# Performance work log

Hardware: AMD Instinct MI355X
Metric: run time of the kernel (lower is better)

The kernel has to match this reference:

```python
import jax, jax.numpy as jnp
import numpy as np

B, T, C = 1, 2048, 1024
HS = 64
H = C // HS
EPS_GN = 0.00064


def _fwd(x, v_first, x_prev, init_state, x_r, x_w, x_k, x_v, x_a, x_g,
         w0, w1, w2, a0, a1, a2, v0, v1, v2, g1, g2,
         k_k, k_a, r_k, Wr, Wk, Wv, Wo, ln_w, ln_b, cu_seqlens):
    # token shift: previous token, sequence starts replaced by cached state x_prev
    xx = jnp.concatenate([jnp.zeros((1, 1, C), x.dtype), x[:, :-1, :]], axis=1)
    xx = xx.at[0, cu_seqlens[:-1], :].set(x_prev)
    xx = xx - x
    xr = x + xx * x_r
    xw = x + xx * x_w
    xk = x + xx * x_k
    xv = x + xx * x_v
    xa = x + xx * x_a
    xg = x + xx * x_g
    r = xr @ Wr.T
    # log-decay, strictly negative: w = -exp(-softplus(-z) - 0.5)
    w = -jnp.exp(-jax.nn.softplus(-(w0 + jnp.tanh(xw @ w1) @ w2)) - 0.5)
    k = xk @ Wk.T
    v = xv @ Wv.T
    # layer_id != 0: mix toward first-layer value
    v = v + (v_first - v) * jax.nn.sigmoid(v0 + (xv @ v1) @ v2)
    a = jax.nn.sigmoid(a0 + (xa @ a1) @ a2)
    g = jax.nn.sigmoid(xg @ g1) @ g2
    kk = (k * k_k).reshape(B, T, H, HS)
    kk = kk / jnp.maximum(jnp.linalg.norm(kk, axis=-1, keepdims=True), 1e-12)
    k = k * (1.0 + (a - 1.0) * k_a)
    r4 = r.reshape(B, T, H, HS)
    w4 = w.reshape(B, T, H, HS)
    k4 = k.reshape(B, T, H, HS)
    v4 = v.reshape(B, T, H, HS)
    a4 = a.reshape(B, T, H, HS)
    aa = -kk
    bb = kk * a4

    # RWKV-7 selective-decay linear RNN (chunk_rwkv7 semantics):
    #   S_t = S_{t-1} diag(exp(w_t)) + (S_{t-1} a_t) b_t^T + v_t k_t^T ; o_t = S_t r_t
    def step(S, ts):
        r_t, w_t, k_t, v_t, a_t, b_t = ts  # each [H,HS]
        sa = jnp.einsum('hvj,hj->hv', S, a_t)
        S = S * jnp.exp(w_t)[:, None, :] + sa[:, :, None] * b_t[:, None, :] \
            + v_t[:, :, None] * k_t[:, None, :]
        o = jnp.einsum('hvk,hk->hv', S, r_t)
        return S, o

    _, y = jax.lax.scan(step, init_state, (r4[0], w4[0], k4[0], v4[0], aa[0], bb[0]))
    # GroupNorm with num_groups=H over channels, eps=0.00064
    y = y.reshape(B * T, H, HS)
    mu = y.mean(-1, keepdims=True)
    var = ((y - mu) ** 2).mean(-1, keepdims=True)
    yn = (y - mu) / jnp.sqrt(var + EPS_GN)
    yn = yn * ln_w.reshape(H, HS) + ln_b.reshape(H, HS)
    xo = yn.reshape(B, T, C)
    # per-head bonus term
    xo = xo + ((r4 * k4 * r_k).sum(-1, keepdims=True) * v4).reshape(B, T, C)
    return (xo * g) @ Wo.T


def setup_inputs():
    keys = jax.random.split(jax.random.key(0), 32)
    it = iter(range(32))
    def nrm(shape, s=0.02):
        return jax.random.normal(keys[next(it)], shape, dtype=jnp.float32) * s
    inp = {}
    inp['x'] = jax.random.normal(keys[next(it)], (B, T, C), jnp.float32)
    inp['v_first'] = jax.random.normal(keys[next(it)], (B, T, C), jnp.float32)
    inp['x_prev'] = jax.random.normal(keys[next(it)], (1, C), jnp.float32)
    inp['init_state'] = jnp.zeros((H, HS, HS), jnp.float32)
    for nm in ['x_r', 'x_w', 'x_k', 'x_v', 'x_a', 'x_g', 'w0', 'a0', 'v0', 'k_k', 'k_a']:
        inp[nm] = nrm((C,))
    inp['w1'] = nrm((C, 64)); inp['w2'] = nrm((64, C))
    inp['a1'] = nrm((C, 64)); inp['a2'] = nrm((64, C))
    inp['v1'] = nrm((C, 32)); inp['v2'] = nrm((32, C))
    inp['g1'] = nrm((C, 128)); inp['g2'] = nrm((128, C))
    inp['r_k'] = nrm((H, HS))
    inp['Wr'] = nrm((C, C)); inp['Wk'] = nrm((C, C))
    inp['Wv'] = nrm((C, C)); inp['Wo'] = nrm((C, C))
    inp['ln_w'] = jnp.ones((C,), jnp.float32)
    inp['ln_b'] = jnp.zeros((C,), jnp.float32)
    inp['cu_seqlens'] = jnp.array([0, T], dtype=jnp.int32)
    return inp


def reference(x, v_first, x_prev, init_state, x_r, x_w, x_k, x_v, x_a, x_g,
              w0, w1, w2, a0, a1, a2, v0, v1, v2, g1, g2,
              k_k, k_a, r_k, Wr, Wk, Wv, Wo, ln_w, ln_b, cu_seqlens):
    return _fwd(x, v_first, x_prev, init_state, x_r, x_w, x_k, x_v, x_a, x_g,
                w0, w1, w2, a0, a1, a2, v0, v1, v2, g1, g2,
                k_k, k_a, r_k, Wr, Wk, Wv, Wo, ln_w, ln_b, cu_seqlens)
```

## Files before the change

### kernel.cpp

```cpp
#include <hip/hip_runtime.h>

#define T_LEN 2048
#define C_DIM 1024
#define PAIR_F 768
#define NCH 32
#define CPAIR 32

#define AS1 __attribute__((address_space(1)))
#define AS3 __attribute__((address_space(3)))

typedef __attribute__((ext_vector_type(8))) short bf8_t;
typedef __attribute__((ext_vector_type(4))) float f4_t;
typedef __attribute__((ext_vector_type(2))) float f2_t;

static __device__ __forceinline__ float sigf(float x) {
    return 1.f / (1.f + __expf(-x));
}
static __device__ __forceinline__ unsigned short f2bf(float f) {
    unsigned u = __float_as_uint(f);
    u += 0x7fff + ((u >> 16) & 1);
    return (unsigned short)(u >> 16);
}

static __device__ __forceinline__ float red16(float x) {
    int xi;
    xi = __builtin_amdgcn_mov_dpp(__float_as_int(x), 0x128, 0xf, 0xf, true);
    x += __int_as_float(xi);
    xi = __builtin_amdgcn_mov_dpp(__float_as_int(x), 0x124, 0xf, 0xf, true);
    x += __int_as_float(xi);
    xi = __builtin_amdgcn_mov_dpp(__float_as_int(x), 0x122, 0xf, 0xf, true);
    x += __int_as_float(xi);
    xi = __builtin_amdgcn_mov_dpp(__float_as_int(x), 0x121, 0xf, 0xf, true);
    x += __int_as_float(xi);
    return x;
}
static __device__ __forceinline__ float red64(float x) {
    x = red16(x);
    x += __shfl_xor(x, 16);
    x += __shfl_xor(x, 32);
    return x;
}

static __device__ __forceinline__ f2_t f2bc(float s) { return (f2_t){s, s}; }
static __device__ __forceinline__ f2_t fma2(f2_t a, f2_t b, f2_t c) {
    return __builtin_elementwise_fma(a, b, c);
}
static __device__ __forceinline__ f2_t lo2(const float4& v) { return (f2_t){v.x, v.y}; }
static __device__ __forceinline__ f2_t hi2(const float4& v) { return (f2_t){v.z, v.w}; }

static __device__ __forceinline__ float dot4pk(f2_t Sl, f2_t Sh, const float4& A) {
    f2_t m = Sl * lo2(A);
    m = fma2(Sh, hi2(A), m);
    return m.x + m.y;
}

__global__ __launch_bounds__(256) void wcvtall(
    const float* __restrict__ Wr, const float* __restrict__ Wk,
    const float* __restrict__ Wv, const float* __restrict__ Wo,
    const float* __restrict__ w1, const float* __restrict__ a1,
    const float* __restrict__ v1, const float* __restrict__ g1,
    const float* __restrict__ g2,
    unsigned short* __restrict__ dst, unsigned short* __restrict__ lw16,
    unsigned short* __restrict__ g2t16)
{
    const int b = blockIdx.x;
    if (b < 4096) {
        const size_t idx = ((size_t)b * 256 + threadIdx.x) * 4;
        const int sel = (int)(idx >> 20);
        const float* src = sel == 0 ? Wr : sel == 1 ? Wk : sel == 2 ? Wv : Wo;
        float4 v = *(const float4*)(src + (idx & 0xFFFFF));
        ushort4 o = {f2bf(v.x), f2bf(v.y), f2bf(v.z), f2bf(v.w)};
        *(ushort4*)(dst + idx) = o;
        return;
    }
    if (b >= 4384) {
        const int rr = b - 4384;
        const int i  = rr * 2 + (threadIdx.x >> 7);
        const int c  = threadIdx.x & 127;
        g2t16[(size_t)i * 128 + c] = f2bf(g2[(size_t)c * C_DIM + i]);
        return;
    }
    const int row = b - 4096;
    const float* src; int Kh, i; unsigned short* dl;
    if (row < 64)       { src = w1; Kh = 64;  i = row;       dl = lw16 + (size_t)row * 1024; }
    else if (row < 128) { src = a1; Kh = 64;  i = row - 64;  dl = lw16 + (size_t)row * 1024; }
    else if (row < 160) { src = v1; Kh = 32;  i = row - 128; dl = lw16 + (size_t)(row - 128 + 128) * 1024; }
    else                { src = g1; Kh = 128; i = row - 160; dl = lw16 + (size_t)(row - 160 + 192) * 1024; }
    const int c0 = threadIdx.x * 4;
#pragma unroll
    for (int u = 0; u < 4; ++u)
        dl[c0 + u] = f2bf(src[(size_t)(c0 + u) * Kh + i]);
}

__global__ __launch_bounds__(256) void xcvt(
    const float* __restrict__ x, const float* __restrict__ xprev,
    const float* __restrict__ x_r, const float* __restrict__ x_k,
    const float* __restrict__ x_v, const float* __restrict__ x_w,
    const float* __restrict__ x_a, const float* __restrict__ x_g,
    unsigned short* __restrict__ xr16, unsigned short* __restrict__ xk16,
    unsigned short* __restrict__ xv16, unsigned short* __restrict__ xw16,
    unsigned short* __restrict__ xa16, unsigned short* __restrict__ xg16)
{
    const int t = blockIdx.x;
    const int c0 = threadIdx.x * 4;
    const size_t base = (size_t)t * C_DIM + c0;
    float4 xv = *(const float4*)(x + base);
    float4 pv = (t == 0) ? *(const float4*)(xprev + c0)
                         : *(const float4*)(x + base - C_DIM);
    float4 dx = {pv.x - xv.x, pv.y - xv.y, pv.z - xv.z, pv.w - xv.w};
#define MIXOUT(mixp, dstp)                                                    \
    {                                                                          \
        float4 mv = *(const float4*)(mixp + c0);                               \
        ushort4 o = {f2bf(xv.x + dx.x * mv.x), f2bf(xv.y + dx.y * mv.y),       \
                     f2bf(xv.z + dx.z * mv.z), f2bf(xv.w + dx.w * mv.w)};      \
        *(ushort4*)(dstp + base) = o;                                          \
    }
    MIXOUT(x_r, xr16) MIXOUT(x_k, xk16) MIXOUT(x_v, xv16)
    MIXOUT(x_w, xw16) MIXOUT(x_a, xa16) MIXOUT(x_g, xg16)
#undef MIXOUT
}

static __device__ __forceinline__ void gemm_core(
    const unsigned short* __restrict__ A, const unsigned short* __restrict__ W,
    float* __restrict__ out)
{
    __shared__ unsigned short Ab[2][128 * 32];
    __shared__ unsigned short Bb[2][64 * 32];
    const int tid = threadIdx.x;
    const int lane = tid & 63;
    const int w = tid >> 6;
    const int n0 = blockIdx.x * 64;
    const int t0 = blockIdx.y * 128;
    const int wm = (w & 1) * 64;
    const int wn = (w >> 1) * 32;
    const int srow = lane >> 2;
    const int scol = (lane & 3) * 8;

    f4_t acc[4][2];
#pragma unroll
    for (int i = 0; i < 4; ++i)
#pragma unroll
        for (int j = 0; j < 2; ++j)
            acc[i][j] = (f4_t){0.f, 0.f, 0.f, 0.f};

#pragma unroll
    for (int s = 0; s < 2; ++s) {
        const int i = 2 * w + s;
        __builtin_amdgcn_global_load_lds(
            (const AS1 unsigned int*)(A + (size_t)(t0 + i * 16 + srow) * 1024 + scol),
            (AS3 unsigned int*)(&Ab[0][i * 512 + lane * 8]), 16, 0, 0);
    }
    __builtin_amdgcn_global_load_lds(
        (const AS1 unsigned int*)(W + (size_t)(n0 + w * 16 + srow) * 1024 + scol),
        (AS3 unsigned int*)(&Bb[0][w * 512 + lane * 8]), 16, 0, 0);

    const int mrow = lane & 15;
    const int kq = (lane >> 4) * 8;
    for (int k0 = 0; k0 < 1024; k0 += 32) {
        const int cur = (k0 >> 5) & 1, nxt = cur ^ 1;
        __syncthreads();
        if (k0 + 32 < 1024) {
            const int k1 = k0 + 32;
#pragma unroll
            for (int s = 0; s < 2; ++s) {
                const int i = 2 * w + s;
                __builtin_amdgcn_global_load_lds(
                    (const AS1 unsigned int*)(A + (size_t)(t0 + i * 16 + srow) * 1024 + k1 + scol),
                    (AS3 unsigned int*)(&Ab[nxt][i * 512 + lane * 8]), 16, 0, 0);
            }
            __builtin_amdgcn_global_load_lds(
                (const AS1 unsigned int*)(W + (size_t)(n0 + w * 16 + srow) * 1024 + k1 + scol),
                (AS3 unsigned int*)(&Bb[nxt][w * 512 + lane * 8]), 16, 0, 0);
        }
        bf8_t af[4], bfr[2];
#pragma unroll
        for (int i = 0; i < 4; ++i)
            af[i] = *(const bf8_t*)(&Ab[cur][(wm + 16 * i + mrow) * 32 + kq]);
#pragma unroll
        for (int j = 0; j < 2; ++j)
            bfr[j] = *(const bf8_t*)(&Bb[cur][(wn + 16 * j + mrow) * 32 + kq]);
#pragma unroll
        for (int i = 0; i < 4; ++i)
#pragma unroll
            for (int j = 0; j < 2; ++j)
                acc[i][j] = __builtin_amdgcn_mfma_f32_16x16x32_bf16(
                    af[i], bfr[j], acc[i][j], 0, 0, 0);
    }
    const int crow = (lane >> 4) * 4;
    const int ccol = lane & 15;
#pragma unroll
    for (int i = 0; i < 4; ++i)
#pragma unroll
        for (int j = 0; j < 2; ++j)
#pragma unroll
            for (int u = 0; u < 4; ++u)
                out[(size_t)(t0 + wm + 16 * i + crow + u) * 1024
                    + n0 + wn + 16 * j + ccol] = acc[i][j][u];
}

__global__ __launch_bounds__(256) void gemm_bf16_3(
    const unsigned short* __restrict__ xr, const unsigned short* __restrict__ xk,
    const unsigned short* __restrict__ xv,
    const unsigned short* __restrict__ Wr, const unsigned short* __restrict__ Wk,
    const unsigned short* __restrict__ Wv,
    float* __restrict__ rB, float* __restrict__ kB, float* __restrict__ vB)
{
    const int z = blockIdx.z;
    const unsigned short* A = z == 0 ? xr : z == 1 ? xk : xv;
    const unsigned short* W = z == 0 ? Wr : z == 1 ? Wk : Wv;
    float* out = z == 0 ? rB : z == 1 ? kB : vB;
    gemm_core(A, W, out);
}

__global__ __launch_bounds__(256) void gemm_bf16(
    const unsigned short* __restrict__ A, const unsigned short* __restrict__ W,
    float* __restrict__ out)
{
    gemm_core(A, W, out);
}

__global__ __launch_bounds__(256) void gemm_g(
    const unsigned short* __restrict__ A, const unsigned short* __restrict__ W,
    float* __restrict__ out)
{
    __shared__ unsigned short Ab[2][128 * 32];
    __shared__ unsigned short Bb[2][64 * 32];
    const int tid = threadIdx.x;
    const int lane = tid & 63;
    const int w = tid >> 6;
    const int n0 = blockIdx.x * 64;
    const int t0 = blockIdx.y * 128;
    const int wm = (w & 1) * 64;
    const int wn = (w >> 1) * 32;
    const int srow = lane >> 2;
    const int scol = (lane & 3) * 8;

    f4_t acc[4][2];
#pragma unroll
    for (int i = 0; i < 4; ++i)
#pragma unroll
        for (int j = 0; j < 2; ++j)
            acc[i][j] = (f4_t){0.f, 0.f, 0.f, 0.f};

#pragma unroll
    for (int s = 0; s < 2; ++s) {
        const int i = 2 * w + s;
        __builtin_amdgcn_global_load_lds(
            (const AS1 unsigned int*)(A + (size_t)(t0 + i * 16 + srow) * 128 + scol),
            (AS3 unsigned int*)(&Ab[0][i * 512 + lane * 8]), 16, 0, 0);
    }
    __builtin_amdgcn_global_load_lds(
        (const AS1 unsigned int*)(W + (size_t)(n0 + w * 16 + srow) * 128 + scol),
        (AS3 unsigned int*)(&Bb[0][w * 512 + lane * 8]), 16, 0, 0);

    const int mrow = lane & 15;
    const int kq = (lane >> 4) * 8;
    for (int k0 = 0; k0 < 128; k0 += 32) {
        const int cur = (k0 >> 5) & 1, nxt = cur ^ 1;
        __syncthreads();
        if (k0 + 32 < 128) {
            const int k1 = k0 + 32;
#pragma unroll
            for (int s = 0; s < 2; ++s) {
                const int i = 2 * w + s;
                __builtin_amdgcn_global_load_lds(
                    (const AS1 unsigned int*)(A + (size_t)(t0 + i * 16 + srow) * 128 + k1 + scol),
                    (AS3 unsigned int*)(&Ab[nxt][i * 512 + lane * 8]), 16, 0, 0);
            }
            __builtin_amdgcn_global_load_lds(
                (const AS1 unsigned int*)(W + (size_t)(n0 + w * 16 + srow) * 128 + k1 + scol),
                (AS3 unsigned int*)(&Bb[nxt][w * 512 + lane * 8]), 16, 0, 0);
        }
        bf8_t af[4], bfr[2];
#pragma unroll
        for (int i = 0; i < 4; ++i)
            af[i] = *(const bf8_t*)(&Ab[cur][(wm + 16 * i + mrow) * 32 + kq]);
#pragma unroll
        for (int j = 0; j < 2; ++j)
            bfr[j] = *(const bf8_t*)(&Bb[cur][(wn + 16 * j + mrow) * 32 + kq]);
#pragma unroll
        for (int i = 0; i < 4; ++i)
#pragma unroll
            for (int j = 0; j < 2; ++j)
                acc[i][j] = __builtin_amdgcn_mfma_f32_16x16x32_bf16(
                    af[i], bfr[j], acc[i][j], 0, 0, 0);
    }
    const int crow = (lane >> 4) * 4;
    const int ccol = lane & 15;
#pragma unroll
    for (int i = 0; i < 4; ++i)
#pragma unroll
        for (int j = 0; j < 2; ++j)
#pragma unroll
            for (int u = 0; u < 4; ++u)
                out[(size_t)(t0 + wm + 16 * i + crow + u) * 1024
                    + n0 + wn + 16 * j + ccol] = acc[i][j][u];
}

__global__ __launch_bounds__(256) void lora1m(
    const unsigned short* __restrict__ xw, const unsigned short* __restrict__ xa,
    const unsigned short* __restrict__ xv, const unsigned short* __restrict__ xg,
    const unsigned short* __restrict__ lw16,
    float* __restrict__ hw, float* __restrict__ ha, float* __restrict__ hv,
    unsigned short* __restrict__ hg16)
{
    const int z = blockIdx.z;
    const unsigned short* A = z == 0 ? xw : z == 1 ? xa : z == 2 ? xv : xg;
    const unsigned short* W = lw16 + (size_t)(z == 0 ? 0 : z == 1 ? 64 : z == 2 ? 128 : 192) * 1024;
    float* out = z == 0 ? hw : z == 1 ? ha : hv;
    const int N  = z == 3 ? 128 : z == 2 ? 32 : 64;
    const int Ns = z == 3 ? 128 : 64;
    const int n0 = blockIdx.x * 64;
    if (n0 >= Ns) return;

    __shared__ unsigned short Ab[2][128 * 32];
    __shared__ unsigned short Bb[2][64 * 32];
    const int tid = threadIdx.x;
    const int lane = tid & 63;
    const int w = tid >> 6;
    const int t0 = blockIdx.y * 128;
    const int wm = (w & 1) * 64;
    const int wn = (w >> 1) * 32;
    const int srow = lane >> 2;
    const int scol = (lane & 3) * 8;

    f4_t acc[4][2];
#pragma unroll
    for (int i = 0; i < 4; ++i)
#pragma unroll
        for (int j = 0; j < 2; ++j)
            acc[i][j] = (f4_t){0.f, 0.f, 0.f, 0.f};

#pragma unroll
    for (int s = 0; s < 2; ++s) {
        const int i = 2 * w + s;
        __builtin_amdgcn_global_load_lds(
            (const AS1 unsigned int*)(A + (size_t)(t0 + i * 16 + srow) * 1024 + scol),
            (AS3 unsigned int*)(&Ab[0][i * 512 + lane * 8]), 16, 0, 0);
    }
    __builtin_amdgcn_global_load_lds(
        (const AS1 unsigned int*)(W + (size_t)(n0 + w * 16 + srow) * 1024 + scol),
        (AS3 unsigned int*)(&Bb[0][w * 512 + lane * 8]), 16, 0, 0);

    const int mrow = lane & 15;
    const int kq = (lane >> 4) * 8;
    for (int k0 = 0; k0 < 1024; k0 += 32) {
        const int cur = (k0 >> 5) & 1, nxt = cur ^ 1;
        __syncthreads();
        if (k0 + 32 < 1024) {
            const int k1 = k0 + 32;
#pragma unroll
            for (int s = 0; s < 2; ++s) {
                const int i = 2 * w + s;
                __builtin_amdgcn_global_load_lds(
                    (const AS1 unsigned int*)(A + (size_t)(t0 + i * 16 + srow) * 1024 + k1 + scol),
                    (AS3 unsigned int*)(&Ab[nxt][i * 512 + lane * 8]), 16, 0, 0);
            }
            __builtin_amdgcn_global_load_lds(
                (const AS1 unsigned int*)(W + (size_t)(n0 + w * 16 + srow) * 1024 + k1 + scol),
                (AS3 unsigned int*)(&Bb[nxt][w * 512 + lane * 8]), 16, 0, 0);
        }
        bf8_t af[4], bfr[2];
#pragma unroll
        for (int i = 0; i < 4; ++i)
            af[i] = *(const bf8_t*)(&Ab[cur][(wm + 16 * i + mrow) * 32 + kq]);
#pragma unroll
        for (int j = 0; j < 2; ++j)
            bfr[j] = *(const bf8_t*)(&Bb[cur][(wn + 16 * j + mrow) * 32 + kq]);
#pragma unroll
        for (int i = 0; i < 4; ++i)
#pragma unroll
            for (int j = 0; j < 2; ++j)
                acc[i][j] = __builtin_amdgcn_mfma_f32_16x16x32_bf16(
                    af[i], bfr[j], acc[i][j], 0, 0, 0);
    }
    const int crow = (lane >> 4) * 4;
    const int ccol = lane & 15;
#pragma unroll
    for (int i = 0; i < 4; ++i)
#pragma unroll
        for (int j = 0; j < 2; ++j) {
            const int col = n0 + wn + 16 * j + ccol;
            if (col < N) {
#pragma unroll
                for (int u = 0; u < 4; ++u) {
                    float vv = acc[i][j][u];
                    if (z == 0) {
                        vv = tanhf(vv);
                        out[(size_t)(t0 + wm + 16 * i + crow + u) * N + col] = vv;
                    } else if (z == 3) {
                        vv = sigf(vv);
                        hg16[(size_t)(t0 + wm + 16 * i + crow + u) * 128 + col] = f2bf(vv);
                    } else {
                        out[(size_t)(t0 + wm + 16 * i + crow + u) * N + col] = vv;
                    }
                }
            }
        }
}

#define TOK 4
__global__ __launch_bounds__(256) void lora2f(
    const float* __restrict__ hwB, const float* __restrict__ haB,
    const float* __restrict__ hvB,
    const float* __restrict__ w2, const float* __restrict__ a2,
    const float* __restrict__ v2,
    const float* __restrict__ w0, const float* __restrict__ a0,
    const float* __restrict__ v0,
    const float* __restrict__ k_k, const float* __restrict__ k_a,
    const float* __restrict__ v_first, const float* __restrict__ rB,
    float* __restrict__ kB, float* __restrict__ vB,
    float* __restrict__ pk)
{
    const int tid = threadIdx.x;
    const int t0 = blockIdx.y * TOK;
    const int i  = blockIdx.x * 256 + tid;
    const int h  = i >> 6;
    const int j  = i & 63;

    float av[TOK], ew[TOK], vf[TOK];
    {
        float acc[TOK];
        const float b0 = a0[i];
#pragma unroll
        for (int tt = 0; tt < TOK; ++tt) acc[tt] = b0;
        for (int jj = 0; jj < 64; jj += 4) {
            const float q0 = a2[(size_t)(jj + 0) * C_DIM + i];
            const float q1 = a2[(size_t)(jj + 1) * C_DIM + i];
            const float q2 = a2[(size_t)(jj + 2) * C_DIM + i];
            const float q3 = a2[(size_t)(jj + 3) * C_DIM + i];
#pragma unroll
            for (int tt = 0; tt < TOK; ++tt) {
                float4 h4 = *(const float4*)(haB + (size_t)(t0 + tt) * 64 + jj);
                acc[tt] = fmaf(h4.x, q0, acc[tt]);
                acc[tt] = fmaf(h4.y, q1, acc[tt]);
                acc[tt] = fmaf(h4.z, q2, acc[tt]);
                acc[tt] = fmaf(h4.w, q3, acc[tt]);
            }
        }
#pragma unroll
        for (int tt = 0; tt < TOK; ++tt) av[tt] = sigf(acc[tt]);
    }
    {
        float acc[TOK];
        const float b0 = w0[i];
#pragma unroll
        for (int tt = 0; tt < TOK; ++tt) acc[tt] = b0;
        for (int jj = 0; jj < 64; jj += 4) {
            const float q0 = w2[(size_t)(jj + 0) * C_DIM + i];
            const float q1 = w2[(size_t)(jj + 1) * C_DIM + i];
            const float q2 = w2[(size_t)(jj + 2) * C_DIM + i];
            const float q3 = w2[(size_t)(jj + 3) * C_DIM + i];
#pragma unroll
            for (int tt = 0; tt < TOK; ++tt) {
                float4 h4 = *(const float4*)(hwB + (size_t)(t0 + tt) * 64 + jj);
                acc[tt] = fmaf(h4.x, q0, acc[tt]);
                acc[tt] = fmaf(h4.y, q1, acc[tt]);
                acc[tt] = fmaf(h4.z, q2, acc[tt]);
                acc[tt] = fmaf(h4.w, q3, acc[tt]);
            }
        }
#pragma unroll
        for (int tt = 0; tt < TOK; ++tt)
            ew[tt] = __expf(-0.6065306597126334f * sigf(acc[tt]));
    }
    {
        float acc[TOK];
        const float b0 = v0[i];
#pragma unroll
        for (int tt = 0; tt < TOK; ++tt) acc[tt] = b0;
        for (int jj = 0; jj < 32; jj += 4) {
            const float q0 = v2[(size_t)(jj + 0) * C_DIM + i];
            const float q1 = v2[(size_t)(jj + 1) * C_DIM + i];
            const float q2 = v2[(size_t)(jj + 2) * C_DIM + i];
            const float q3 = v2[(size_t)(jj + 3) * C_DIM + i];
#pragma unroll
            for (int tt = 0; tt < TOK; ++tt) {
                float4 h4 = *(const float4*)(hvB + (size_t)(t0 + tt) * 32 + jj);
                acc[tt] = fmaf(h4.x, q0, acc[tt]);
                acc[tt] = fmaf(h4.y, q1, acc[tt]);
                acc[tt] = fmaf(h4.z, q2, acc[tt]);
                acc[tt] = fmaf(h4.w, q3, acc[tt]);
            }
        }
#pragma unroll
        for (int tt = 0; tt < TOK; ++tt) {
            const size_t gi = (size_t)(t0 + tt) * C_DIM + i;
            const float s = sigf(acc[tt]);
            const float vr = vB[gi];
            vf[tt] = vr + (v_first[gi] - vr) * s;
            vB[gi] = vf[tt];
        }
    }
    const float kkw = k_k[i], kaw = k_a[i];
    const size_t pbase = (size_t)h * 1024 * PAIR_F;
    for (int pt = 0; pt < TOK / 2; ++pt) {
        float r_[2], e_[2], kf_[2], v_[2], aa_[2], bb_[2];
#pragma unroll
        for (int u = 0; u < 2; ++u) {
            const int tt = 2 * pt + u;
            const size_t gi = (size_t)(t0 + tt) * C_DIM + i;
            const float kraw = kB[gi];
            const float kn = kraw * kkw;
            const float ss = red64(kn * kn);
            const float sc = 1.f / fmaxf(sqrtf(ss), 1e-12f);
            const float kk = kn * sc;
            const float a_ = av[tt];
            const float kf = kraw * (1.f + (a_ - 1.f) * kaw);
            kB[gi] = kf;
            r_[u] = rB[gi];
            e_[u] = ew[tt];
            kf_[u] = kf;
            v_[u] = vf[tt];
            aa_[u] = -kk;
            bb_[u] = kk * a_;
        }
        const float E   = e_[0] * e_[1];
        const float A2e = e_[0] * aa_[1];
        const float B1e = bb_[0] * e_[1];
        const float K1e = kf_[0] * e_[1];
        const float R1e = e_[0] * r_[0];
        const float cba = red64(bb_[0] * aa_[1]);
        const float cka = red64(kf_[0] * aa_[1]);
        const float cbr = red64(bb_[0] * r_[0]);
        const float ckr = red64(kf_[0] * r_[0]);
        const float cbr2  = red64(B1e * r_[1]);
        const float ckr2  = red64(K1e * r_[1]);
        const float cb2r2 = red64(bb_[1] * r_[1]);
        const float ck2r2 = red64(kf_[1] * r_[1]);
        float* p = pk + pbase + (size_t)(blockIdx.y * (TOK / 2) + pt) * PAIR_F;
        p[j]        = E;
        p[64 + j]   = aa_[0];
        p[128 + j]  = A2e;
        p[192 + j]  = B1e;
        p[256 + j]  = K1e;
        p[320 + j]  = bb_[1];
        p[384 + j]  = kf_[1];
        p[448 + j]  = R1e;
        p[512 + j]  = E * r_[1];
        p[576 + 2 * j]     = v_[0];
        p[576 + 2 * j + 1] = v_[1];
        if (j == 0) {
            p[704] = cba;  p[705] = cka;  p[706] = cbr;  p[707] = ckr;
            p[708] = cbr2; p[709] = ckr2; p[710] = cb2r2; p[711] = ck2r2;
        }
    }
}

struct SlotPC {
    float4 E, A1, A2e, B1e, K1e, B2, K2;
    float4 vva, vvb;
    float4 sc;
};

static __device__ __forceinline__ void slot_load_pc(
    SlotPC& K, const float* __restrict__ p, int j0, int rb2)
{
    K.E   = *(const float4*)(p + j0);
    K.A1  = *(const float4*)(p + 64 + j0);
    K.A2e = *(const float4*)(p + 128 + j0);
    K.B1e = *(const float4*)(p + 192 + j0);
    K.K1e = *(const float4*)(p + 256 + j0);
    K.B2  = *(const float4*)(p + 320 + j0);
    K.K2  = *(const float4*)(p + 384 + j0);
    K.vva = *(const float4*)(p + 576 + rb2);
    K.vvb = *(const float4*)(p + 576 + rb2 + 4);
    K.sc  = *(const float4*)(p + 704);
}

static __device__ __forceinline__ void pair_pc(
    f2_t* PSl, f2_t* PSh, f2_t* CSl, f2_t* CSh, const SlotPC& K)
{
    float pu1[4], pu2[4], cu1[4], cu2[4];
#pragma unroll
    for (int r = 0; r < 4; ++r) {
        pu1[r] = red16(dot4pk(PSl[r], PSh[r], K.A1));
        pu2[r] = red16(dot4pk(PSl[r], PSh[r], K.A2e));
        cu1[r] = red16(dot4pk(CSl[r], CSh[r], K.A1));
        cu2[r] = red16(dot4pk(CSl[r], CSh[r], K.A2e));
    }
#pragma unroll
    for (int r = 0; r < 4; ++r) {
        {
            const float sa1 = pu1[r];
            const float sa2 = fmaf(sa1, K.sc.x, pu2[r]);
            const f2_t sa1v = f2bc(sa1), sa2v = f2bc(sa2);
            f2_t nl = PSl[r] * lo2(K.E), nh = PSh[r] * hi2(K.E);
            nl = fma2(sa1v, lo2(K.B1e), nl); nh = fma2(sa1v, hi2(K.B1e), nh);
            nl = fma2(sa2v, lo2(K.B2), nl);  nh = fma2(sa2v, hi2(K.B2), nh);
            PSl[r] = nl; PSh[r] = nh;
        }
        {
            const float v1 = r == 0 ? K.vva.x : r == 1 ? K.vva.z
                           : r == 2 ? K.vvb.x : K.vvb.z;
            const float v2 = r == 0 ? K.vva.y : r == 1 ? K.vva.w
                           : r == 2 ? K.vvb.y : K.vvb.w;
            const float sa1 = cu1[r];
            const float sa2 = fmaf(v1, K.sc.y, fmaf(sa1, K.sc.x, cu2[r]));
            const f2_t sa1v = f2bc(sa1), sa2v = f2bc(sa2);
            const f2_t v1v = f2bc(v1), v2v = f2bc(v2);
            f2_t nl = CSl[r] * lo2(K.E), nh = CSh[r] * hi2(K.E);
            nl = fma2(sa1v, lo2(K.B1e), nl); nh = fma2(sa1v, hi2(K.B1e), nh);
            nl = fma2(v1v, lo2(K.K1e), nl);  nh = fma2(v1v, hi2(K.K1e), nh);
            nl = fma2(sa2v, lo2(K.B2), nl);  nh = fma2(sa2v, hi2(K.B2), nh);
            nl = fma2(v2v, lo2(K.K2), nl);   nh = fma2(v2v, hi2(K.K2), nh);
            CSl[r] = nl; CSh[r] = nh;
        }
    }
}

__global__ __launch_bounds__(64, 1) void pc_fused(
    const float* __restrict__ pk, float* __restrict__ Pbuf,
    float* __restrict__ Cbuf)
{
    const int b = blockIdx.x;
    const int h = b & 15;
    const int w = (b >> 4) & 3;
    const int c = b >> 6;
    const int l = threadIdx.x;
    const int q = l >> 4;
    const int j0 = (l & 15) * 4;
    const int rbase = w * 16 + q * 4;
    const int rb2 = 2 * rbase;
    const float* hbase = pk + ((size_t)h * 1024 + (size_t)c * CPAIR) * PAIR_F;

    f2_t PSl[4], PSh[4], CSl[4], CSh[4];
#pragma unroll
    for (int r = 0; r < 4; ++r) {
        const int row = rbase + r;
        PSl[r] = (f2_t){j0 == row ? 1.f : 0.f, j0 + 1 == row ? 1.f : 0.f};
        PSh[r] = (f2_t){j0 + 2 == row ? 1.f : 0.f, j0 + 3 == row ? 1.f : 0.f};
        CSl[r] = (f2_t){0.f, 0.f};
        CSh[r] = (f2_t){0.f, 0.f};
    }

    SlotPC s0, s1, s2, s3;
    slot_load_pc(s0, hbase + 0 * PAIR_F, j0, rb2);
    slot_load_pc(s1, hbase + 1 * PAIR_F, j0, rb2);
    slot_load_pc(s2, hbase + 2 * PAIR_F, j0, rb2);
    slot_load_pc(s3, hbase + 3 * PAIR_F, j0, rb2);
    __builtin_amdgcn_sched_barrier(0);

    for (int i = 0; i < CPAIR - 4; i += 4) {
        const float* pl = hbase + (size_t)(i + 4) * PAIR_F;
        pair_pc(PSl, PSh, CSl, CSh, s0); slot_load_pc(s0, pl + 0 * PAIR_F, j0, rb2);
        __builtin_amdgcn_sched_barrier(0);
        pair_pc(PSl, PSh, CSl, CSh, s1); slot_load_pc(s1, pl + 1 * PAIR_F, j0, rb2);
        __builtin_amdgcn_sched_barrier(0);
        pair_pc(PSl, PSh, CSl, CSh, s2); slot_load_pc(s2, pl + 2 * PAIR_F, j0, rb2);
        __builtin_amdgcn_sched_barrier(0);
        pair_pc(PSl, PSh, CSl, CSh, s3); slot_load_pc(s3, pl + 3 * PAIR_F, j0, rb2);
        __builtin_amdgcn_sched_barrier(0);
    }
    pair_pc(PSl, PSh, CSl, CSh, s0);
    pair_pc(PSl, PSh, CSl, CSh, s1);
    pair_pc(PSl, PSh, CSl, CSh, s2);
    pair_pc(PSl, PSh, CSl, CSh, s3);

    const size_t cb64 = ((size_t)h * NCH + c) * 4096;
#pragma unroll
    for (int r = 0; r < 4; ++r) {
        *(float4*)(Pbuf + cb64 + (size_t)(rbase + r) * 64 + j0) =
            (float4){PSl[r].x, PSl[r].y, PSh[r].x, PSh[r].y};
        *(float4*)(Cbuf + cb64 + (size_t)(rbase + r) * 64 + j0) =
            (float4){CSl[r].x, CSl[r].y, CSh[r].x, CSh[r].y};
    }
}

__global__ __launch_bounds__(64) void combine(
    const float* __restrict__ Pbuf, float* __restrict__ CSbuf,
    const float* __restrict__ init_state)
{
    const int b = blockIdx.x;
    const int h = b & 15;
    const int g = b >> 4;
    const int l = threadIdx.x;
    const int vl = l >> 4;
    const int vidx = g * 4 + vl;
    const int j0 = (l & 15) * 4;
    __shared__ __align__(16) float Pl[64 * 64];
    __shared__ __align__(16) float sl[4 * 64];

    float4 s = *(const float4*)(init_state + h * 4096 + vidx * 64 + j0);
    for (int c = 0; c < NCH; ++c) {
        const size_t cbase = ((size_t)h * NCH + c) * 4096;
        float* cp = CSbuf + cbase + (size_t)vidx * 64 + j0;
        float4 Cv = *(const float4*)cp;
        *(float4*)cp = s;
        const float* Psrc = Pbuf + cbase;
#pragma unroll
        for (int t = 0; t < 16; ++t)
            *(float4*)(&Pl[t * 256 + l * 4]) = *(const float4*)(Psrc + t * 256 + l * 4);
        *(float4*)(&sl[vl * 64 + j0]) = s;
        __syncthreads();
        f2_t al = {Cv.x, Cv.y}, ah = {Cv.z, Cv.w};
        for (int k = 0; k < 64; ++k) {
            const float sk = sl[vl * 64 + k];
            float4 Pr = *(const float4*)(&Pl[k * 64 + j0]);
            al = fma2(f2bc(sk), lo2(Pr), al);
            ah = fma2(f2bc(sk), hi2(Pr), ah);
        }
        s = (float4){al.x, al.y, ah.x, ah.y};
        __syncthreads();
    }
}

struct SlotO {
    float4 E, A1, A2e, B1e, K1e, B2, K2, R1e, R2e;
    float4 vva, vvb;
    float4 sc, sc2;
};

static __device__ __forceinline__ void slot_load_o(
    SlotO& K, const float* __restrict__ p, int j0, int rb2)
{
    K.E   = *(const float4*)(p + j0);
    K.A1  = *(const float4*)(p + 64 + j0);
    K.A2e = *(const float4*)(p + 128 + j0);
    K.B1e = *(const float4*)(p + 192 + j0);
    K.K1e = *(const float4*)(p + 256 + j0);
    K.B2  = *(const float4*)(p + 320 + j0);
    K.K2  = *(const float4*)(p + 384 + j0);
    K.R1e = *(const float4*)(p + 448 + j0);
    K.R2e = *(const float4*)(p + 512 + j0);
    K.vva = *(const float4*)(p + 576 + rb2);
    K.vvb = *(const float4*)(p + 576 + rb2 + 4);
    K.sc  = *(const float4*)(p + 704);
    K.sc2 = *(const float4*)(p + 708);
}

static __device__ __forceinline__ void pair_out(
    f2_t* Sl, f2_t* Sh, const SlotO& K, float4& o1v, float4& o2v)
{
    float u1[4], u2[4], op[4], oz[4];
#pragma unroll
    for (int r = 0; r < 4; ++r) {
        u1[r] = red16(dot4pk(Sl[r], Sh[r], K.A1));
        u2[r] = red16(dot4pk(Sl[r], Sh[r], K.A2e));
        op[r] = red16(dot4pk(Sl[r], Sh[r], K.R1e));
        oz[r] = red16(dot4pk(Sl[r], Sh[r], K.R2e));
    }
    float o1a[4], o2a[4];
#pragma unroll
    for (int r = 0; r < 4; ++r) {
        const float v1 = r == 0 ? K.vva.x : r == 1 ? K.vva.z
                       : r == 2 ? K.vvb.x : K.vvb.z;
        const float v2 = r == 0 ? K.vva.y : r == 1 ? K.vva.w
                       : r == 2 ? K.vvb.y : K.vvb.w;
        const float sa1 = u1[r];
        const float sa2 = fmaf(v1, K.sc.y, fmaf(sa1, K.sc.x, u2[r]));
        o1a[r] = fmaf(v1, K.sc.w, fmaf(sa1, K.sc.z, op[r]));
        o2a[r] = fmaf(v2, K.sc2.w, fmaf(sa2, K.sc2.z,
                 fmaf(v1, K.sc2.y, fmaf(sa1, K.sc2.x, oz[r]))));
        const f2_t sa1v = f2bc(sa1), sa2v = f2bc(sa2);
        const f2_t v1v = f2bc(v1), v2v = f2bc(v2);
        f2_t nl = Sl[r] * lo2(K.E), nh = Sh[r] * hi2(K.E);
        nl = fma2(sa1v, lo2(K.B1e), nl); nh = fma2(sa1v, hi2(K.B1e), nh);
        nl = fma2(v1v, lo2(K.K1e), nl);  nh = fma2(v1v, hi2(K.K1e), nh);
        nl = fma2(sa2v, lo2(K.B2), nl);  nh = fma2(sa2v, hi2(K.B2), nh);
        nl = fma2(v2v, lo2(K.K2), nl);   nh = fma2(v2v, hi2(K.K2), nh);
        Sl[r] = nl; Sh[r] = nh;
    }
    o1v = (float4){o1a[0], o1a[1], o1a[2], o1a[3]};
    o2v = (float4){o2a[0], o2a[1], o2a[2], o2a[3]};
}

__global__ __launch_bounds__(64, 1) void out_scan(
    const float* __restrict__ pk, const float* __restrict__ Scbuf,
    float* __restrict__ y)
{
    const int b = blockIdx.x;
    const int h = b & 15;
    const int w = (b >> 4) & 3;
    const int c = b >> 6;
    const int l = threadIdx.x;
    const int q = l >> 4;
    const int j0 = (l & 15) * 4;
    const int rbase = w * 16 + q * 4;
    const int rb2 = 2 * rbase;
    const int cb = h * 64;
    const float* hbase = pk + ((size_t)h * 1024 + (size_t)c * CPAIR) * PAIR_F;
    const size_t cb64 = ((size_t)h * NCH + c) * 4096;

    f2_t Sl[4], Sh[4];
#pragma unroll
    for (int r = 0; r < 4; ++r) {
        float4 S4 = *(const float4*)(Scbuf + cb64 + (size_t)(rbase + r) * 64 + j0);
        Sl[r] = (f2_t){S4.x, S4.y};
        Sh[r] = (f2_t){S4.z, S4.w};
    }

    SlotO s0, s1;
    slot_load_o(s0, hbase + 0 * PAIR_F, j0, rb2);
    slot_load_o(s1, hbase + 1 * PAIR_F, j0, rb2);
    __builtin_amdgcn_sched_barrier(0);

    const bool wr = (l & 15) == 0;
    const int pi0 = c * CPAIR;
    float4 o1v, o2v;
#define OUT_STORE(pidx)                                                       \
    if (wr) {                                                                 \
        float* yp = y + (size_t)(2 * (pidx)) * C_DIM + cb + rbase;            \
        *(float4*)yp = o1v;                                                   \
        *(float4*)(yp + C_DIM) = o2v;                                         \
    }
    for (int i = 0; i < CPAIR - 2; i += 2) {
        pair_out(Sl, Sh, s0, o1v, o2v);
        slot_load_o(s0, hbase + (size_t)(i + 2) * PAIR_F, j0, rb2);
        __builtin_amdgcn_sched_barrier(0);
        OUT_STORE(pi0 + i)
        pair_out(Sl, Sh, s1, o1v, o2v);
        if (i + 3 < CPAIR)
            slot_load_o(s1, hbase + (size_t)(i + 3) * PAIR_F, j0, rb2);
        __builtin_amdgcn_sched_barrier(0);
        OUT_STORE(pi0 + i + 1)
    }
    pair_out(Sl, Sh, s0, o1v, o2v);
    OUT_STORE(pi0 + CPAIR - 2)
    pair_out(Sl, Sh, s1, o1v, o2v);
    OUT_STORE(pi0 + CPAIR - 1)
#undef OUT_STORE
}

__global__ __launch_bounds__(256) void gn_bonus(
    const float* __restrict__ y, const float* __restrict__ rb,
    const float* __restrict__ kb, const float* __restrict__ vb,
    const float* __restrict__ gb, const float* __restrict__ r_k,
    const float* __restrict__ lnw, const float* __restrict__ lnb,
    unsigned short* __restrict__ yg)
{
    const int t = blockIdx.x, tid = threadIdx.x;
    const int c0 = tid << 2;
    const size_t base = (size_t)t * C_DIM + c0;
    float4 yv = *(const float4*)(y + base);
    float sum = yv.x + yv.y + yv.z + yv.w;
    float ss  = yv.x * yv.x + yv.y * yv.y + yv.z * yv.z + yv.w * yv.w;
    float4 rv = *(const float4*)(rb + base);
    float4 kv = *(const float4*)(kb + base);
    float4 rkv = *(const float4*)(r_k + c0);
    float dot = rv.x * kv.x * rkv.x + rv.y * kv.y * rkv.y +
                rv.z * kv.z * rkv.z + rv.w * kv.w * rkv.w;
#pragma unroll
    for (int m = 1; m <= 8; m <<= 1) {
        sum += __shfl_xor(sum, m);
        ss  += __shfl_xor(ss, m);
        dot += __shfl_xor(dot, m);
    }
    const float mu = sum * 0.015625f;
    const float var = ss * 0.015625f - mu * mu;
    const float rstd = rsqrtf(var + 0.00064f);
    float4 wv = *(const float4*)(lnw + c0);
    float4 bv = *(const float4*)(lnb + c0);
    float4 vv = *(const float4*)(vb + base);
    float4 gv = *(const float4*)(gb + base);
    ushort4 o;
    o.x = f2bf(((yv.x - mu) * rstd * wv.x + bv.x + dot * vv.x) * gv.x);
    o.y = f2bf(((yv.y - mu) * rstd * wv.y + bv.y + dot * vv.y) * gv.y);
    o.z = f2bf(((yv.z - mu) * rstd * wv.z + bv.z + dot * vv.z) * gv.z);
    o.w = f2bf(((yv.w - mu) * rstd * wv.w + bv.w + dot * vv.w) * gv.w);
    *(ushort4*)(yg + base) = o;
}

extern "C" void kernel_launch(void* const* d_in, const int* in_sizes, int n_in,
                              void* d_out, int out_size, void* d_ws, size_t ws_size,
                              hipStream_t stream)
{
    (void)in_sizes; (void)n_in; (void)out_size; (void)ws_size;
    const float* x       = (const float*)d_in[0];
    const float* v_first = (const float*)d_in[1];
    const float* x_prev  = (const float*)d_in[2];
    const float* init_st = (const float*)d_in[3];
    const float* x_r = (const float*)d_in[4];
    const float* x_w = (const float*)d_in[5];
    const float* x_k = (const float*)d_in[6];
    const float* x_v = (const float*)d_in[7];
    const float* x_a = (const float*)d_in[8];
    const float* x_g = (const float*)d_in[9];
    const float* w0  = (const float*)d_in[10];
    const float* a0  = (const float*)d_in[11];
    const float* v0  = (const float*)d_in[12];
    const float* k_k = (const float*)d_in[13];
    const float* k_a = (const float*)d_in[14];
    const float* w1  = (const float*)d_in[15];
    const float* w2  = (const float*)d_in[16];
    const float* a1  = (const float*)d_in[17];
    const float* a2  = (const float*)d_in[18];
    const float* v1  = (const float*)d_in[19];
    const float* v2  = (const float*)d_in[20];
    const float* g1  = (const float*)d_in[21];
    const float* g2  = (const float*)d_in[22];
    const float* r_k = (const float*)d_in[23];
    const float* Wr  = (const float*)d_in[24];
    const float* Wk  = (const float*)d_in[25];
    const float* Wv  = (const float*)d_in[26];
    const float* Wo  = (const float*)d_in[27];
    const float* ln_w = (const float*)d_in[28];
    const float* ln_b = (const float*)d_in[29];

    float* out = (float*)d_out;
    float* ws  = (float*)d_ws;
    const size_t NE = (size_t)T_LEN * C_DIM;
    const size_t WE = (size_t)C_DIM * C_DIM;
    float* rB  = ws;
    float* kB  = ws + NE;
    float* vB  = ws + 2 * NE;
    float* gB  = ws + 3 * NE;
    float* hwB = ws + 4 * NE;
    float* haB = hwB + (size_t)T_LEN * 64;
    float* hvB = haB + (size_t)T_LEN * 64;
    float* pk  = ws + 4 * NE + NE / 2;
    unsigned short* b16 = (unsigned short*)(ws + 10 * NE + NE / 2);
    unsigned short* xr16 = b16;
    unsigned short* xk16 = b16 + NE;
    unsigned short* xv16 = b16 + 2 * NE;
    unsigned short* Wr16 = b16 + 3 * NE;
    unsigned short* Wk16 = Wr16 + WE;
    unsigned short* Wv16 = Wr16 + 2 * WE;
    unsigned short* Wo16 = Wr16 + 3 * WE;
    unsigned short* yg16 = b16 + 3 * NE + 4 * WE;
    unsigned short* lw16 = yg16 + NE;
    unsigned short* hg16 = lw16 + (size_t)320 * 1024;
    unsigned short* g2t16 = hg16 + (size_t)T_LEN * 128;
    unsigned short* xw16 = (unsigned short*)pk;
    unsigned short* xa16 = xw16 + NE;
    unsigned short* xg16 = xw16 + 2 * NE;
    float* yB = (float*)xr16;
    float* Pbuf  = (float*)xr16;
    float* CSbuf = (float*)xv16;

    wcvtall<<<4896, 256, 0, stream>>>(Wr, Wk, Wv, Wo, w1, a1, v1, g1, g2,
                                      Wr16, lw16, g2t16);
    xcvt<<<T_LEN, 256, 0, stream>>>(x, x_prev, x_r, x_k, x_v, x_w, x_a, x_g,
                                    xr16, xk16, xv16, xw16, xa16, xg16);

    gemm_bf16_3<<<dim3(16, 16, 3), 256, 0, stream>>>(
        xr16, xk16, xv16, Wr16, Wk16, Wv16, rB, kB, vB);

    lora1m<<<dim3(2, 16, 4), 256, 0, stream>>>(
        xw16, xa16, xv16, xg16, lw16, hwB, haB, hvB, hg16);

    gemm_g<<<dim3(16, 16), 256, 0, stream>>>(hg16, g2t16, gB);

    lora2f<<<dim3(4, T_LEN / TOK), 256, 0, stream>>>(
        hwB, haB, hvB, w2, a2, v2, w0, a0, v0,
        k_k, k_a, v_first, rB, kB, vB, pk);

    pc_fused<<<16 * 4 * NCH, 64, 0, stream>>>(pk, Pbuf, CSbuf);
    combine<<<256, 64, 0, stream>>>(Pbuf, CSbuf, init_st);
    out_scan<<<16 * 4 * NCH, 64, 0, stream>>>(pk, CSbuf, yB);

    gn_bonus<<<T_LEN, 256, 0, stream>>>(yB, rB, kB, vB, gB, r_k, ln_w, ln_b, yg16);
    gemm_bf16<<<dim3(16, 16), 256, 0, stream>>>(yg16, Wo16, out);
}
```

Before: 369.4 us.

## Move a/v LoRA up-projections from scalar FMA loops onto bf16 MFMA GEMM

```diff
diff --git a/kernel.cpp b/kernel.cpp
--- a/kernel.cpp
+++ b/kernel.cpp
@@ -20,6 +20,9 @@
     unsigned u = __float_as_uint(f);
     u += 0x7fff + ((u >> 16) & 1);
     return (unsigned short)(u >> 16);
+}
+static __device__ __forceinline__ float bf2f(unsigned short u) {
+    return __uint_as_float(((unsigned)u) << 16);
 }
 
 static __device__ __forceinline__ float red16(float x) {
@@ -59,9 +62,11 @@
     const float* __restrict__ Wv, const float* __restrict__ Wo,
     const float* __restrict__ w1, const float* __restrict__ a1,
     const float* __restrict__ v1, const float* __restrict__ g1,
-    const float* __restrict__ g2,
+    const float* __restrict__ g2, const float* __restrict__ a2,
+    const float* __restrict__ v2,
     unsigned short* __restrict__ dst, unsigned short* __restrict__ lw16,
-    unsigned short* __restrict__ g2t16)
+    unsigned short* __restrict__ g2t16, unsigned short* __restrict__ a2t16,
+    unsigned short* __restrict__ v2t16)
 {
     const int b = blockIdx.x;
     if (b < 4096) {
@@ -71,6 +76,26 @@
         float4 v = *(const float4*)(src + (idx & 0xFFFFF));
         ushort4 o = {f2bf(v.x), f2bf(v.y), f2bf(v.z), f2bf(v.w)};
         *(ushort4*)(dst + idx) = o;
+        return;
+    }
+    if (b >= 4960) {
+        const int rr = b - 4960;
+        const int e  = rr * 1024 + threadIdx.x * 4;
+        const int i  = e >> 5;
+        const int c  = e & 31;
+#pragma unroll
+        for (int u = 0; u < 4; ++u)
+            v2t16[(size_t)i * 32 + c + u] = f2bf(v2[(size_t)(c + u) * C_DIM + i]);
+        return;
+    }
+    if (b >= 4896) {
+        const int rr = b - 4896;
+        const int e  = rr * 1024 + threadIdx.x * 4;
+        const int i  = e >> 6;
+        const int c  = e & 63;
+#pragma unroll
+        for (int u = 0; u < 4; ++u)
+            a2t16[(size_t)i * 64 + c + u] = f2bf(a2[(size_t)(c + u) * C_DIM + i]);
         return;
     }
     if (b >= 4384) {
@@ -297,17 +322,106 @@
                     + n0 + wn + 16 * j + ccol] = acc[i][j][u];
 }
 
+__global__ __launch_bounds__(256) void gemm_av(
+    const unsigned short* __restrict__ ha16, const unsigned short* __restrict__ a2t,
+    const unsigned short* __restrict__ hv16, const unsigned short* __restrict__ v2t,
+    const float* __restrict__ a0, const float* __restrict__ v0,
+    unsigned short* __restrict__ av16, unsigned short* __restrict__ vs16)
+{
+    const int z = blockIdx.z;
+    const unsigned short* A = z ? hv16 : ha16;
+    const unsigned short* W = z ? v2t : a2t;
+    const float* bias = z ? v0 : a0;
+    unsigned short* out = z ? vs16 : av16;
+    const int Kr = z ? 32 : 64;
+
+    __shared__ unsigned short Ab[2][128 * 32];
+    __shared__ unsigned short Bb[2][64 * 32];
+    const int tid = threadIdx.x;
+    const int lane = tid & 63;
+    const int w = tid >> 6;
+    const int n0 = blockIdx.x * 64;
+    const int t0 = blockIdx.y * 128;
+    const int wm = (w & 1) * 64;
+    const int wn = (w >> 1) * 32;
+    const int srow = lane >> 2;
+    const int scol = (lane & 3) * 8;
+
+    f4_t acc[4][2];
+#pragma unroll
+    for (int i = 0; i < 4; ++i)
+#pragma unroll
+        for (int j = 0; j < 2; ++j)
+            acc[i][j] = (f4_t){0.f, 0.f, 0.f, 0.f};
+
+#pragma unroll
+    for (int s = 0; s < 2; ++s) {
+        const int i = 2 * w + s;
+        __builtin_amdgcn_global_load_lds(
+            (const AS1 unsigned int*)(A + (size_t)(t0 + i * 16 + srow) * Kr + scol),
+            (AS3 unsigned int*)(&Ab[0][i * 512 + lane * 8]), 16, 0, 0);
+    }
+    __builtin_amdgcn_global_load_lds(
+        (const AS1 unsigned int*)(W + (size_t)(n0 + w * 16 + srow) * Kr + scol),
+        (AS3 unsigned int*)(&Bb[0][w * 512 + lane * 8]), 16, 0, 0);
+
+    const int mrow = lane & 15;
+    const int kq = (lane >> 4) * 8;
+    for (int k0 = 0; k0 < Kr; k0 += 32) {
+        const int cur = (k0 >> 5) & 1, nxt = cur ^ 1;
+        __syncthreads();
+        if (k0 + 32 < Kr) {
+            const int k1 = k0 + 32;
+#pragma unroll
+            for (int s = 0; s < 2; ++s) {
+                const int i = 2 * w + s;
+                __builtin_amdgcn_global_load_lds(
+                    (const AS1 unsigned int*)(A + (size_t)(t0 + i * 16 + srow) * Kr + k1 + scol),
+                    (AS3 unsigned int*)(&Ab[nxt][i * 512 + lane * 8]), 16, 0, 0);
+            }
+            __builtin_amdgcn_global_load_lds(
+                (const AS1 unsigned int*)(W + (size_t)(n0 + w * 16 + srow) * Kr + k1 + scol),
+                (AS3 unsigned int*)(&Bb[nxt][w * 512 + lane * 8]), 16, 0, 0);
+        }
+        bf8_t af[4], bfr[2];
+#pragma unroll
+        for (int i = 0; i < 4; ++i)
+            af[i] = *(const bf8_t*)(&Ab[cur][(wm + 16 * i + mrow) * 32 + kq]);
+#pragma unroll
+        for (int j = 0; j < 2; ++j)
+            bfr[j] = *(const bf8_t*)(&Bb[cur][(wn + 16 * j + mrow) * 32 + kq]);
+#pragma unroll
+        for (int i = 0; i < 4; ++i)
+#pragma unroll
+            for (int j = 0; j < 2; ++j)
+                acc[i][j] = __builtin_amdgcn_mfma_f32_16x16x32_bf16(
+                    af[i], bfr[j], acc[i][j], 0, 0, 0);
+    }
+    const int crow = (lane >> 4) * 4;
+    const int ccol = lane & 15;
+#pragma unroll
+    for (int i = 0; i < 4; ++i)
+#pragma unroll
+        for (int j = 0; j < 2; ++j) {
+            const int col = n0 + wn + 16 * j + ccol;
+            const float b0 = bias[col];
+#pragma unroll
+            for (int u = 0; u < 4; ++u)
+                out[(size_t)(t0 + wm + 16 * i + crow + u) * 1024 + col] =
+                    f2bf(sigf(acc[i][j][u] + b0));
+        }
+}
+
 __global__ __launch_bounds__(256) void lora1m(
     const unsigned short* __restrict__ xw, const unsigned short* __restrict__ xa,
     const unsigned short* __restrict__ xv, const unsigned short* __restrict__ xg,
     const unsigned short* __restrict__ lw16,
-    float* __restrict__ hw, float* __restrict__ ha, float* __restrict__ hv,
-    unsigned short* __restrict__ hg16)
+    float* __restrict__ hw, unsigned short* __restrict__ ha16,
+    unsigned short* __restrict__ hv16, unsigned short* __restrict__ hg16)
 {
     const int z = blockIdx.z;
     const unsigned short* A = z == 0 ? xw : z == 1 ? xa : z == 2 ? xv : xg;
     const unsigned short* W = lw16 + (size_t)(z == 0 ? 0 : z == 1 ? 64 : z == 2 ? 128 : 192) * 1024;
-    float* out = z == 0 ? hw : z == 1 ? ha : hv;
     const int N  = z == 3 ? 128 : z == 2 ? 32 : 64;
     const int Ns = z == 3 ? 128 : 64;
     const int n0 = blockIdx.x * 64;
@@ -384,15 +498,16 @@
             if (col < N) {
 #pragma unroll
                 for (int u = 0; u < 4; ++u) {
+                    const int row = t0 + wm + 16 * i + crow + u;
                     float vv = acc[i][j][u];
                     if (z == 0) {
-                        vv = tanhf(vv);
-                        out[(size_t)(t0 + wm + 16 * i + crow + u) * N + col] = vv;
-                    } else if (z == 3) {
-                        vv = sigf(vv);
-                        hg16[(size_t)(t0 + wm + 16 * i + crow + u) * 128 + col] = f2bf(vv);
+                        hw[(size_t)row * 64 + col] = tanhf(vv);
+                    } else if (z == 1) {
+                        ha16[(size_t)row * 64 + col] = f2bf(vv);
+                    } else if (z == 2) {
+                        hv16[(size_t)row * 32 + col] = f2bf(vv);
                     } else {
-                        out[(size_t)(t0 + wm + 16 * i + crow + u) * N + col] = vv;
+                        hg16[(size_t)row * 128 + col] = f2bf(sigf(vv));
                     }
                 }
             }
@@ -401,12 +516,9 @@
 
 #define TOK 4
 __global__ __launch_bounds__(256) void lora2f(
-    const float* __restrict__ hwB, const float* __restrict__ haB,
-    const float* __restrict__ hvB,
-    const float* __restrict__ w2, const float* __restrict__ a2,
-    const float* __restrict__ v2,
-    const float* __restrict__ w0, const float* __restrict__ a0,
-    const float* __restrict__ v0,
+    const float* __restrict__ hwB,
+    const float* __restrict__ w2, const float* __restrict__ w0,
+    const unsigned short* __restrict__ av16, const unsigned short* __restrict__ vs16,
     const float* __restrict__ k_k, const float* __restrict__ k_a,
     const float* __restrict__ v_first, const float* __restrict__ rB,
     float* __restrict__ kB, float* __restrict__ vB,
@@ -419,28 +531,6 @@
     const int j  = i & 63;
 
     float av[TOK], ew[TOK], vf[TOK];
-    {
-        float acc[TOK];
-        const float b0 = a0[i];
-#pragma unroll
-        for (int tt = 0; tt < TOK; ++tt) acc[tt] = b0;
-        for (int jj = 0; jj < 64; jj += 4) {
-            const float q0 = a2[(size_t)(jj + 0) * C_DIM + i];
-            const float q1 = a2[(size_t)(jj + 1) * C_DIM + i];
-            const float q2 = a2[(size_t)(jj + 2) * C_DIM + i];
-            const float q3 = a2[(size_t)(jj + 3) * C_DIM + i];
-#pragma unroll
-            for (int tt = 0; tt < TOK; ++tt) {
-                float4 h4 = *(const float4*)(haB + (size_t)(t0 + tt) * 64 + jj);
-                acc[tt] = fmaf(h4.x, q0, acc[tt]);
-                acc[tt] = fmaf(h4.y, q1, acc[tt]);
-                acc[tt] = fmaf(h4.z, q2, acc[tt]);
-                acc[tt] = fmaf(h4.w, q3, acc[tt]);
-            }
-        }
-#pragma unroll
-        for (int tt = 0; tt < TOK; ++tt) av[tt] = sigf(acc[tt]);
-    }
     {
         float acc[TOK];
         const float b0 = w0[i];
@@ -465,28 +555,11 @@
             ew[tt] = __expf(-0.6065306597126334f * sigf(acc[tt]));
     }
     {
-        float acc[TOK];
-        const float b0 = v0[i];
-#pragma unroll
-        for (int tt = 0; tt < TOK; ++tt) acc[tt] = b0;
-        for (int jj = 0; jj < 32; jj += 4) {
-            const float q0 = v2[(size_t)(jj + 0) * C_DIM + i];
-            const float q1 = v2[(size_t)(jj + 1) * C_DIM + i];
-            const float q2 = v2[(size_t)(jj + 2) * C_DIM + i];
-            const float q3 = v2[(size_t)(jj + 3) * C_DIM + i];
-#pragma unroll
-            for (int tt = 0; tt < TOK; ++tt) {
-                float4 h4 = *(const float4*)(hvB + (size_t)(t0 + tt) * 32 + jj);
-                acc[tt] = fmaf(h4.x, q0, acc[tt]);
-                acc[tt] = fmaf(h4.y, q1, acc[tt]);
-                acc[tt] = fmaf(h4.z, q2, acc[tt]);
-                acc[tt] = fmaf(h4.w, q3, acc[tt]);
-            }
-        }
 #pragma unroll
         for (int tt = 0; tt < TOK; ++tt) {
             const size_t gi = (size_t)(t0 + tt) * C_DIM + i;
-            const float s = sigf(acc[tt]);
+            av[tt] = bf2f(av16[gi]);
+            const float s = bf2f(vs16[gi]);
             const float vr = vB[gi];
             vf[tt] = vr + (v_first[gi] - vr) * s;
             vB[gi] = vf[tt];
@@ -906,8 +979,6 @@
     float* vB  = ws + 2 * NE;
     float* gB  = ws + 3 * NE;
     float* hwB = ws + 4 * NE;
-    float* haB = hwB + (size_t)T_LEN * 64;
-    float* hvB = haB + (size_t)T_LEN * 64;
     float* pk  = ws + 4 * NE + NE / 2;
     unsigned short* b16 = (unsigned short*)(ws + 10 * NE + NE / 2);
     unsigned short* xr16 = b16;
@@ -921,6 +992,12 @@
     unsigned short* lw16 = yg16 + NE;
     unsigned short* hg16 = lw16 + (size_t)320 * 1024;
     unsigned short* g2t16 = hg16 + (size_t)T_LEN * 128;
+    unsigned short* a2t16 = g2t16 + (size_t)128 * 1024;
+    unsigned short* v2t16 = a2t16 + (size_t)64 * 1024;
+    unsigned short* ha16 = Wv16;
+    unsigned short* hv16 = Wv16 + (size_t)T_LEN * 64;
+    unsigned short* av16 = yg16;
+    unsigned short* vs16 = xr16;
     unsigned short* xw16 = (unsigned short*)pk;
     unsigned short* xa16 = xw16 + NE;
     unsigned short* xg16 = xw16 + 2 * NE;
@@ -928,8 +1005,8 @@
     float* Pbuf  = (float*)xr16;
     float* CSbuf = (float*)xv16;
 
-    wcvtall<<<4896, 256, 0, stream>>>(Wr, Wk, Wv, Wo, w1, a1, v1, g1, g2,
-                                      Wr16, lw16, g2t16);
+    wcvtall<<<4992, 256, 0, stream>>>(Wr, Wk, Wv, Wo, w1, a1, v1, g1, g2, a2, v2,
+                                      Wr16, lw16, g2t16, a2t16, v2t16);
     xcvt<<<T_LEN, 256, 0, stream>>>(x, x_prev, x_r, x_k, x_v, x_w, x_a, x_g,
                                     xr16, xk16, xv16, xw16, xa16, xg16);
 
@@ -937,12 +1014,14 @@
         xr16, xk16, xv16, Wr16, Wk16, Wv16, rB, kB, vB);
 
     lora1m<<<dim3(2, 16, 4), 256, 0, stream>>>(
-        xw16, xa16, xv16, xg16, lw16, hwB, haB, hvB, hg16);
+        xw16, xa16, xv16, xg16, lw16, hwB, ha16, hv16, hg16);
 
     gemm_g<<<dim3(16, 16), 256, 0, stream>>>(hg16, g2t16, gB);
+    gemm_av<<<dim3(16, 16, 2), 256, 0, stream>>>(
+        ha16, a2t16, hv16, v2t16, a0, v0, av16, vs16);
 
     lora2f<<<dim3(4, T_LEN / TOK), 256, 0, stream>>>(
-        hwB, haB, hvB, w2, a2, v2, w0, a0, v0,
+        hwB, w2, w0, av16, vs16,
         k_k, k_a, v_first, rB, kB, vB, pk);
 
     pc_fused<<<16 * 4 * NCH, 64, 0, stream>>>(pk, Pbuf, CSbuf);
```

Measured after the change: 376.8 us. Within noise of the previous version (+2.0%).
